# Performance work log

Measured on AMD Instinct MI355X. Metric: run time of the kernel, lower is better.

The kernel has to match this reference:

```python
import jax, jax.numpy as jnp
import numpy as np

NUM_GRAPHS = 256


def _mean_aggregate(h, src, dst, num_nodes):
    # DGL copy_src + mean reduce: dst node gets mean of src-node features over in-edges.
    summed = jax.ops.segment_sum(h[src], dst, num_segments=num_nodes)  # [N, F]
    deg = jax.ops.segment_sum(jnp.ones((src.shape[0],), h.dtype), dst, num_segments=num_nodes)
    return summed / jnp.maximum(deg, 1.0)[:, None]


def setup_inputs() -> dict:
    key = jax.random.key(0)
    ks = jax.random.split(key, 10)
    N, E, D_IN, H1, H2, OUT = 50000, 800000, 128, 256, 128, 1
    s = lambda fan: 1.0 / np.sqrt(fan)
    return {
        "h": jax.random.normal(ks[0], (N, D_IN), jnp.float32),
        "src": jax.random.randint(ks[1], (E,), 0, N),
        "dst": jax.random.randint(ks[2], (E,), 0, N),
        "graph_ids": jnp.sort(jax.random.randint(ks[3], (N,), 0, NUM_GRAPHS)),
        "W1": jax.random.normal(ks[4], (D_IN, H1), jnp.float32) * s(D_IN),
        "b1": jnp.zeros((H1,), jnp.float32),
        "W2": jax.random.normal(ks[5], (H1, H1), jnp.float32) * s(H1),
        "b2": jnp.zeros((H1,), jnp.float32),
        "Wr1": jax.random.normal(ks[6], (H1, H2), jnp.float32) * s(H1),
        "br1": jnp.zeros((H2,), jnp.float32),
        "Wr2": jax.random.normal(ks[7], (H2, OUT), jnp.float32) * s(H2),
        "br2": jnp.zeros((OUT,), jnp.float32),
    }


def reference(h, src, dst, graph_ids, W1, b1, W2, b2, Wr1, br1, Wr2, br2):
    N = h.shape[0]
    # GCN layer 1: mean-aggregate then linear+ReLU
    h = _mean_aggregate(h, src, dst, N)
    h = jax.nn.relu(h @ W1 + b1)
    # GCN layer 2
    h = _mean_aggregate(h, src, dst, N)
    h = jax.nn.relu(h @ W2 + b2)
    # dgl.mean_nodes readout: per-graph mean of node features
    gsum = jax.ops.segment_sum(h, graph_ids, num_segments=NUM_GRAPHS)  # [G, H1]
    gcnt = jax.ops.segment_sum(jnp.ones((N,), h.dtype), graph_ids, num_segments=NUM_GRAPHS)
    hg = gsum / jnp.maximum(gcnt, 1.0)[:, None]
    hidden = hg @ Wr1 + br1
    return hidden @ Wr2 + br2  # [G, 1]
```

## Files before the change

### kernel.cpp

```cpp
#include <hip/hip_runtime.h>


#define NUM_GRAPHS 256
#define MAXDEG 64
#define GSHIFT 9
#define GCAP 9216

#define PART_B0 0
#define PART_NB 256
#define CST_B0 (PART_B0 + PART_NB)
#define CST_NB 512
#define GST_B0 (CST_B0 + CST_NB)
#define GST_NB 64
#define WT1_B0 (GST_B0 + GST_NB)
#define WT1_NB 16
#define WT2_B0 (WT1_B0 + WT1_NB)
#define WT2_NB 32
#define MISC_NB (WT2_B0 + WT2_NB)

typedef __attribute__((ext_vector_type(8))) short bf16x8;
typedef __attribute__((ext_vector_type(4))) float f32x4;

__device__ inline unsigned short f2bf(float f) {
    unsigned u = __float_as_uint(f);
    return (unsigned short)((u + 0x7fff + ((u >> 16) & 1)) >> 16);
}
__device__ inline float bflo(unsigned u) { return __uint_as_float(u << 16); }
__device__ inline float bfhi(unsigned u) { return __uint_as_float(u & 0xffff0000u); }


__launch_bounds__(256)
__global__ void misc_kernel(const int* __restrict__ dst, const int* __restrict__ src,
                            const int* __restrict__ gids,
                            const float* __restrict__ h,
                            const float* __restrict__ W1, const float* __restrict__ W2,
                            int* __restrict__ cursor, unsigned* __restrict__ partE,
                            int* __restrict__ gstart,
                            unsigned short* __restrict__ hb,
                            unsigned short* __restrict__ Wt1, unsigned short* __restrict__ Wt2,
                            int N, int E) {
    int b = blockIdx.x, tid = threadIdx.x;
    if (b < CST_B0) {
        __shared__ unsigned lcnt[128];
        __shared__ unsigned gb[128];
        int ngrp = (N + 511) >> GSHIFT;
        int b0 = b - PART_B0;
        int chunk = (E + PART_NB - 1) / PART_NB;
        int ebeg = b0 * chunk;
        int eend = ebeg + chunk; if (eend > E) eend = E;
        for (int i = tid; i < 128; i += 256) lcnt[i] = 0;
        __syncthreads();
        for (int e = ebeg + tid; e < eend; e += 256) {
            int d = __builtin_nontemporal_load(&dst[e]);
            atomicAdd(&lcnt[d >> GSHIFT], 1u);
        }
        __syncthreads();
        for (int g = tid; g < ngrp; g += 256) {
            unsigned c = lcnt[g];
            gb[g] = c ? (unsigned)atomicAdd(&cursor[g], (int)c) : 0u;
            lcnt[g] = 0;
        }
        __syncthreads();
        for (int e = ebeg + tid; e < eend; e += 256) {
            int d = __builtin_nontemporal_load(&dst[e]);
            int s = __builtin_nontemporal_load(&src[e]);
            int g = d >> GSHIFT;
            unsigned r = atomicAdd(&lcnt[g], 1u) + gb[g];
            if (r < GCAP)
                __builtin_nontemporal_store(((unsigned)s << GSHIFT) | (unsigned)(d & 511),
                                            &partE[(size_t)g * GCAP + r]);
        }
    } else if (b < GST_B0) {
        int lid = (b - CST_B0) * 256 + tid;
        int total4 = N * 32;
        for (int i = lid; i < total4; i += CST_NB * 256) {
            float4 v = *(const float4*)(h + (size_t)i * 4);
            ushort4 o;
            o.x = f2bf(v.x); o.y = f2bf(v.y); o.z = f2bf(v.z); o.w = f2bf(v.w);
            *(ushort4*)(hb + (size_t)i * 4) = o;
        }
    } else if (b < WT1_B0) {
        int lid = (b - GST_B0) * 256 + tid;
        for (int n = lid; n < N; n += GST_NB * 256) {
            int g = gids[n];
            int gp = (n == 0) ? -1 : gids[n - 1];
            for (int x = gp + 1; x <= g; ++x) gstart[x] = n;
            if (n == N - 1)
                for (int x = g + 1; x <= NUM_GRAPHS; ++x) gstart[x] = N;
        }
    } else if (b < WT2_B0) {
        int lid = (b - WT1_B0) * 256 + tid;
        for (int i = lid; i < 256 * 128; i += WT1_NB * 256)
            Wt1[i] = f2bf(W1[(size_t)(i & 127) * 256 + (i >> 7)]);
    } else {
        int lid = (b - WT2_B0) * 256 + tid;
        for (int i = lid; i < 256 * 256; i += WT2_NB * 256)
            Wt2[i] = f2bf(W2[(size_t)(i & 255) * 256 + (i >> 8)]);
    }
}


__launch_bounds__(256)
__global__ void build_kernel(const unsigned* __restrict__ partE,
                             const int* __restrict__ cursor,
                             int* __restrict__ cnt, unsigned short* __restrict__ eidx,
                             int N) {
    __shared__ unsigned hist[512];
    int g = blockIdx.x, tid = threadIdx.x;
    for (int i = tid; i < 512; i += 256) hist[i] = 0;
    __syncthreads();
    int ec = cursor[g]; if (ec > GCAP) ec = GCAP;
    const unsigned* pe = partE + (size_t)g * GCAP;
    for (int i = tid; i < ec; i += 256) {
        unsigned p = pe[i];
        int dl = (int)(p & 511);
        int s = (int)(p >> GSHIFT);
        unsigned r = atomicAdd(&hist[dl], 1u);
        if (r < MAXDEG)
            eidx[((size_t)((g << GSHIFT) + dl)) * MAXDEG + r] = (unsigned short)s;
    }
    __syncthreads();
    for (int i = tid; i < 512; i += 256) {
        int node = (g << GSHIFT) + i;
        if (node < N) cnt[node] = (int)hist[i];
    }
}


template <int D>
__global__ void agg_mean_bf16_kernel(const unsigned short* __restrict__ feat,
                                     const int* __restrict__ cnt,
                                     const unsigned short* __restrict__ eidx,
                                     unsigned short* __restrict__ out, int N) {
    constexpr int VPL = D / 64;
    int wave = blockIdx.x * (blockDim.x >> 6) + (threadIdx.x >> 6);
    int lane = threadIdx.x & 63;
    if (wave >= N) return;
    int deg = cnt[wave];
    int stored = deg > MAXDEG ? MAXDEG : deg;
    const unsigned short* row = eidx + (size_t)wave * MAXDEG;
    int myIdx = (lane < stored) ? (int)row[lane] : 0;

    float acc[VPL];
    #pragma unroll
    for (int i = 0; i < VPL; ++i) acc[i] = 0.0f;

    int j = 0;
    for (; j + 8 <= stored; j += 8) {
        if constexpr (VPL == 2) {
            unsigned v[8];
            #pragma unroll
            for (int u = 0; u < 8; ++u) {
                int s = __shfl(myIdx, j + u, 64);
                v[u] = *(const unsigned*)(feat + (size_t)s * D + lane * 2);
            }
            #pragma unroll
            for (int u = 0; u < 8; ++u) { acc[0] += bflo(v[u]); acc[1] += bfhi(v[u]); }
        } else {
            uint2 v[8];
            #pragma unroll
            for (int u = 0; u < 8; ++u) {
                int s = __shfl(myIdx, j + u, 64);
                v[u] = *(const uint2*)(feat + (size_t)s * D + lane * 4);
            }
            #pragma unroll
            for (int u = 0; u < 8; ++u) {
                acc[0] += bflo(v[u].x); acc[1] += bfhi(v[u].x);
                acc[2] += bflo(v[u].y); acc[3] += bfhi(v[u].y);
            }
        }
    }
    for (; j < stored; ++j) {
        int s = __shfl(myIdx, j, 64);
        if constexpr (VPL == 2) {
            unsigned v = *(const unsigned*)(feat + (size_t)s * D + lane * 2);
            acc[0] += bflo(v); acc[1] += bfhi(v);
        } else {
            uint2 v = *(const uint2*)(feat + (size_t)s * D + lane * 4);
            acc[0] += bflo(v.x); acc[1] += bfhi(v.x);
            acc[2] += bflo(v.y); acc[3] += bfhi(v.y);
        }
    }

    float invd = 1.0f / (float)(deg > 0 ? deg : 1);
    if constexpr (VPL == 2) {
        unsigned o = (unsigned)f2bf(acc[0] * invd) | ((unsigned)f2bf(acc[1] * invd) << 16);
        __builtin_nontemporal_store(o, (unsigned*)(out + (size_t)wave * D + lane * 2));
    } else {
        unsigned lo = (unsigned)f2bf(acc[0] * invd) | ((unsigned)f2bf(acc[1] * invd) << 16);
        unsigned hi = (unsigned)f2bf(acc[2] * invd) | ((unsigned)f2bf(acc[3] * invd) << 16);
        unsigned long long o = (unsigned long long)lo | ((unsigned long long)hi << 32);
        __builtin_nontemporal_store(o, (unsigned long long*)(out + (size_t)wave * D + lane * 4));
    }
}


template <int K, int MODE>
__launch_bounds__(256)
__global__ void gemm_mfma_kernel(const unsigned short* __restrict__ A,
                                 const unsigned short* __restrict__ Wt,
                                 const float* __restrict__ bias,
                                 unsigned short* __restrict__ Cb,
                                 const int* __restrict__ gids,
                                 float* __restrict__ gsum,
                                 int N) {
    constexpr int LDS = 40;
    __shared__ unsigned short As[64 * LDS];
    __shared__ unsigned short Bs[256 * LDS];

    int tid = threadIdx.x;
    int wave = tid >> 6;
    int lane = tid & 63;
    int m = lane & 15;
    int q = lane >> 4;
    int rowBase = blockIdx.x * 64;

    f32x4 acc[4][4] = {};

    for (int kc = 0; kc < K; kc += 32) {
        {
            int r = tid >> 2;
            int seg = tid & 3;
            int gr = rowBase + r;
            uint4 v = make_uint4(0, 0, 0, 0);
            if (gr < N) v = *(const uint4*)(A + (size_t)gr * K + kc + seg * 8);
            *(uint4*)&As[r * LDS + seg * 8] = v;
        }
        #pragma unroll
        for (int it = 0; it < 4; ++it) {
            int n = (tid >> 2) + it * 64;
            int seg = tid & 3;
            uint4 v = *(const uint4*)(Wt + (size_t)n * K + kc + seg * 8);
            *(uint4*)&Bs[n * LDS + seg * 8] = v;
        }
        __syncthreads();

        bf16x8 af[4], bfr[4];
        #pragma unroll
        for (int r = 0; r < 4; ++r)
            af[r] = *(const bf16x8*)&As[(r * 16 + m) * LDS + q * 8];
        #pragma unroll
        for (int c = 0; c < 4; ++c)
            bfr[c] = *(const bf16x8*)&Bs[(wave * 64 + c * 16 + m) * LDS + q * 8];
        #pragma unroll
        for (int r = 0; r < 4; ++r)
            #pragma unroll
            for (int c = 0; c < 4; ++c)
                acc[r][c] = __builtin_amdgcn_mfma_f32_16x16x32_bf16(af[r], bfr[c], acc[r][c], 0, 0, 0);
        __syncthreads();
    }

    if constexpr (MODE == 0) {
        #pragma unroll
        for (int c = 0; c < 4; ++c) {
            int col = wave * 64 + c * 16 + m;
            float bv = bias[col];
            #pragma unroll
            for (int r = 0; r < 4; ++r) {
                #pragma unroll
                for (int reg = 0; reg < 4; ++reg) {
                    int grow = rowBase + r * 16 + q * 4 + reg;
                    if (grow < N)
                        Cb[(size_t)grow * 256 + col] = f2bf(fmaxf(acc[r][c][reg] + bv, 0.0f));
                }
            }
        }
    } else {
        int* sgid = (int*)As;
        if (tid < 64) {
            int gr = rowBase + tid;
            sgid[tid] = (gr < N) ? gids[gr] : 0x7fffffff;
        }
        __syncthreads();
        int lastValid = N - 1 - rowBase;
        if (lastValid > 63) lastValid = 63;
        int gmin = sgid[0];
        int gmax = sgid[lastValid];
        #pragma unroll
        for (int c = 0; c < 4; ++c) {
            int col = wave * 64 + c * 16 + m;
            float bv = bias[col];
            for (int g = gmin; g <= gmax; ++g) {
                float p = 0.0f;
                #pragma unroll
                for (int r = 0; r < 4; ++r) {
                    #pragma unroll
                    for (int reg = 0; reg < 4; ++reg) {
                        int lr = r * 16 + q * 4 + reg;
                        if (sgid[lr] == g)
                            p += fmaxf(acc[r][c][reg] + bv, 0.0f);
                    }
                }
                p += __shfl_xor(p, 16, 64);
                p += __shfl_xor(p, 32, 64);
                if (q == 0 && p != 0.0f)
                    atomicAdd(&gsum[g * 256 + col], p);
            }
        }
    }
}


__global__ void final_kernel(const float* __restrict__ gsum, const int* __restrict__ gstart,
                             const float* __restrict__ Wr1, const float* __restrict__ br1,
                             const float* __restrict__ Wr2, const float* __restrict__ br2,
                             float* __restrict__ out) {
    __shared__ float part[512];
    __shared__ float ws2[2];
    int g = blockIdx.x;
    int t = threadIdx.x;
    int j = t & 127;
    int kq = t >> 7;
    int c = gstart[g + 1] - gstart[g];
    float invc = 1.0f / (float)(c > 0 ? c : 1);
    const float* gs = gsum + g * 256;
    float acc = 0.0f;
    #pragma unroll 8
    for (int k = kq * 64; k < kq * 64 + 64; ++k)
        acc += gs[k] * Wr1[k * 128 + j];
    part[t] = acc;
    __syncthreads();
    if (t < 128) {
        float s = part[j] + part[128 + j] + part[256 + j] + part[384 + j];
        float p = (s * invc + br1[j]) * Wr2[j];
        #pragma unroll
        for (int d = 32; d > 0; d >>= 1) p += __shfl_down(p, d, 64);
        if ((t & 63) == 0) ws2[t >> 6] = p;
    }
    __syncthreads();
    if (t == 0) out[g] = ws2[0] + ws2[1] + br2[0];
}


extern "C" void kernel_launch(void* const* d_in, const int* in_sizes, int n_in,
                              void* d_out, int out_size, void* d_ws, size_t ws_size,
                              hipStream_t stream) {
    const float* h    = (const float*)d_in[0];
    const int*   src  = (const int*)d_in[1];
    const int*   dst  = (const int*)d_in[2];
    const int*   gids = (const int*)d_in[3];
    const float* W1   = (const float*)d_in[4];
    const float* b1   = (const float*)d_in[5];
    const float* W2   = (const float*)d_in[6];
    const float* b2   = (const float*)d_in[7];
    const float* Wr1  = (const float*)d_in[8];
    const float* br1  = (const float*)d_in[9];
    const float* Wr2  = (const float*)d_in[10];
    const float* br2  = (const float*)d_in[11];

    int N = in_sizes[0] / 128;
    int E = in_sizes[1];
    int ngrp = (N + 511) >> GSHIFT;

    char* w = (char*)d_ws;
    unsigned short* hb     = (unsigned short*)w;  w += (size_t)N * 128 * sizeof(unsigned short);
    unsigned short* h1b    = (unsigned short*)w;  w += (size_t)N * 256 * sizeof(unsigned short);
    unsigned short* aggOut = (unsigned short*)w;  w += (size_t)N * 256 * sizeof(unsigned short);
    int* cnt    = (int*)w;              w += (size_t)N * sizeof(int);
    float* gsum = (float*)w;            w += (size_t)NUM_GRAPHS * 256 * sizeof(float);
    int* cursor = (int*)w;              w += 128 * sizeof(int);
    unsigned short* eidx = (unsigned short*)w;  w += (size_t)N * MAXDEG * sizeof(unsigned short);
    unsigned short* Wt1 = (unsigned short*)w;   w += 256 * 128 * sizeof(unsigned short);
    unsigned short* Wt2 = (unsigned short*)w;   w += 256 * 256 * sizeof(unsigned short);
    int* gstart = (int*)w;              w += (size_t)(NUM_GRAPHS + 1) * sizeof(int);
    unsigned* partE = (unsigned*)aggOut;

    hipMemsetAsync(gsum, 0,
                   (size_t)NUM_GRAPHS * 256 * sizeof(float) + 128 * sizeof(int),
                   stream);
    misc_kernel<<<MISC_NB, 256, 0, stream>>>(dst, src, gids, h, W1, W2, cursor, partE,
                                             gstart, hb, Wt1, Wt2, N, E);
    build_kernel<<<ngrp, 256, 0, stream>>>(partE, cursor, cnt, eidx, N);

    agg_mean_bf16_kernel<128><<<(N + 3) / 4, 256, 0, stream>>>(hb, cnt, eidx, aggOut, N);
    gemm_mfma_kernel<128, 0><<<(N + 63) / 64, 256, 0, stream>>>(aggOut, Wt1, b1, h1b, nullptr, nullptr, N);

    agg_mean_bf16_kernel<256><<<(N + 3) / 4, 256, 0, stream>>>(h1b, cnt, eidx, aggOut, N);
    gemm_mfma_kernel<256, 1><<<(N + 63) / 64, 256, 0, stream>>>(aggOut, Wt2, b2, nullptr, gids, gsum, N);

    final_kernel<<<NUM_GRAPHS, 512, 0, stream>>>(gsum, gstart, Wr1, br1, Wr2, br2, (float*)d_out);
}
```

Measured before the change: 286.7 us.

## Stage edge partitioning in LDS for coalesced writes and smaller dst groups

The edge partitioning pass now sorts each block's edges by destination group in shared memory, using a prefix scan and a compaction buffer, then writes them out contiguously per group instead of scattering them one by one. Groups shrink from 512 to 256 destination nodes, which doubles the number of build blocks and halves their per-group capacity. The build kernel assembles each group's neighbour lists in LDS and writes them out with vectorised nontemporal stores, replacing scattered 2-byte global writes. In exchange it adds scan barriers, a binary search per edge and 32KB of LDS in the build kernel, which may lower occupancy.

```diff
diff --git a/kernel.cpp b/kernel.cpp
--- a/kernel.cpp
+++ b/kernel.cpp
@@ -3,8 +3,9 @@
 
 #define NUM_GRAPHS 256
 #define MAXDEG 64
-#define GSHIFT 9
-#define GCAP 9216
+#define GSHIFT 8
+#define GCAP 4864
+#define CHUNK_MAX 3200
 
 #define PART_B0 0
 #define PART_NB 256
@@ -20,6 +21,7 @@
 
 typedef __attribute__((ext_vector_type(8))) short bf16x8;
 typedef __attribute__((ext_vector_type(4))) float f32x4;
+typedef __attribute__((ext_vector_type(4))) unsigned int u32x4;
 
 __device__ inline unsigned short f2bf(float f) {
     unsigned u = __float_as_uint(f);
@@ -41,34 +43,57 @@
                             int N, int E) {
     int b = blockIdx.x, tid = threadIdx.x;
     if (b < CST_B0) {
-        __shared__ unsigned lcnt[128];
-        __shared__ unsigned gb[128];
-        int ngrp = (N + 511) >> GSHIFT;
+        __shared__ unsigned lcnt[256];
+        __shared__ unsigned sbuf[256];
+        __shared__ unsigned lbase[257];
+        __shared__ unsigned gb[256];
+        __shared__ unsigned comp[CHUNK_MAX];
         int b0 = b - PART_B0;
         int chunk = (E + PART_NB - 1) / PART_NB;
         int ebeg = b0 * chunk;
         int eend = ebeg + chunk; if (eend > E) eend = E;
-        for (int i = tid; i < 128; i += 256) lcnt[i] = 0;
+        int ecount = eend - ebeg; if (ecount < 0) ecount = 0;
+
+        lcnt[tid] = 0;
         __syncthreads();
         for (int e = ebeg + tid; e < eend; e += 256) {
             int d = __builtin_nontemporal_load(&dst[e]);
             atomicAdd(&lcnt[d >> GSHIFT], 1u);
         }
         __syncthreads();
-        for (int g = tid; g < ngrp; g += 256) {
-            unsigned c = lcnt[g];
-            gb[g] = c ? (unsigned)atomicAdd(&cursor[g], (int)c) : 0u;
-            lcnt[g] = 0;
-        }
+        unsigned v = lcnt[tid];
+        sbuf[tid] = v;
+        __syncthreads();
+        #pragma unroll
+        for (int dd = 1; dd < 256; dd <<= 1) {
+            unsigned t = (tid >= dd) ? sbuf[tid - dd] : 0u;
+            __syncthreads();
+            sbuf[tid] += t;
+            __syncthreads();
+        }
+        lbase[tid] = sbuf[tid] - v;
+        if (tid == 255) lbase[256] = sbuf[255];
+        gb[tid] = v ? (unsigned)atomicAdd(&cursor[tid], (int)v) : 0u;
+        lcnt[tid] = 0;
         __syncthreads();
         for (int e = ebeg + tid; e < eend; e += 256) {
             int d = __builtin_nontemporal_load(&dst[e]);
             int s = __builtin_nontemporal_load(&src[e]);
             int g = d >> GSHIFT;
-            unsigned r = atomicAdd(&lcnt[g], 1u) + gb[g];
-            if (r < GCAP)
-                __builtin_nontemporal_store(((unsigned)s << GSHIFT) | (unsigned)(d & 511),
-                                            &partE[(size_t)g * GCAP + r]);
+            unsigned r = atomicAdd(&lcnt[g], 1u) + lbase[g];
+            if (r < (unsigned)CHUNK_MAX)
+                comp[r] = ((unsigned)s << GSHIFT) | (unsigned)(d & 255);
+        }
+        __syncthreads();
+        for (int i = tid; i < ecount; i += 256) {
+            int lo = 0, hi = 256;
+            while (hi - lo > 1) {
+                int mid = (lo + hi) >> 1;
+                if (lbase[mid] <= (unsigned)i) lo = mid; else hi = mid;
+            }
+            unsigned dest = (unsigned)lo * GCAP + gb[lo] + ((unsigned)i - lbase[lo]);
+            if (dest < (unsigned)(256 * GCAP))
+                __builtin_nontemporal_store(comp[i], &partE[dest]);
         }
     } else if (b < GST_B0) {
         int lid = (b - CST_B0) * 256 + tid;
@@ -105,25 +130,28 @@
                              const int* __restrict__ cursor,
                              int* __restrict__ cnt, unsigned short* __restrict__ eidx,
                              int N) {
-    __shared__ unsigned hist[512];
+    __shared__ unsigned short es[256 * MAXDEG];
+    __shared__ unsigned hist[256];
     int g = blockIdx.x, tid = threadIdx.x;
-    for (int i = tid; i < 512; i += 256) hist[i] = 0;
+    hist[tid] = 0;
     __syncthreads();
     int ec = cursor[g]; if (ec > GCAP) ec = GCAP;
     const unsigned* pe = partE + (size_t)g * GCAP;
     for (int i = tid; i < ec; i += 256) {
         unsigned p = pe[i];
-        int dl = (int)(p & 511);
+        int dl = (int)(p & 255);
         int s = (int)(p >> GSHIFT);
         unsigned r = atomicAdd(&hist[dl], 1u);
         if (r < MAXDEG)
-            eidx[((size_t)((g << GSHIFT) + dl)) * MAXDEG + r] = (unsigned short)s;
+            es[dl * MAXDEG + r] = (unsigned short)s;
     }
     __syncthreads();
-    for (int i = tid; i < 512; i += 256) {
-        int node = (g << GSHIFT) + i;
-        if (node < N) cnt[node] = (int)hist[i];
-    }
+    const u32x4* s4 = (const u32x4*)es;
+    u32x4* d4 = (u32x4*)(eidx + ((size_t)g << GSHIFT) * MAXDEG);
+    for (int i = tid; i < 2048; i += 256)
+        __builtin_nontemporal_store(s4[i], &d4[i]);
+    int node = (g << GSHIFT) + tid;
+    if (node < N) cnt[node] = (int)hist[tid];
 }
 
 
@@ -350,7 +378,7 @@
 
     int N = in_sizes[0] / 128;
     int E = in_sizes[1];
-    int ngrp = (N + 511) >> GSHIFT;
+    int ngrp = (N + 255) >> GSHIFT;
 
     char* w = (char*)d_ws;
     unsigned short* hb     = (unsigned short*)w;  w += (size_t)N * 128 * sizeof(unsigned short);
@@ -358,16 +386,16 @@
     unsigned short* aggOut = (unsigned short*)w;  w += (size_t)N * 256 * sizeof(unsigned short);
     int* cnt    = (int*)w;              w += (size_t)N * sizeof(int);
     float* gsum = (float*)w;            w += (size_t)NUM_GRAPHS * 256 * sizeof(float);
-    int* cursor = (int*)w;              w += 128 * sizeof(int);
-    unsigned short* eidx = (unsigned short*)w;  w += (size_t)N * MAXDEG * sizeof(unsigned short);
+    int* cursor = (int*)w;              w += 256 * sizeof(int);
+    unsigned short* eidx = (unsigned short*)w;  w += (size_t)ngrp * 256 * MAXDEG * sizeof(unsigned short);
     unsigned short* Wt1 = (unsigned short*)w;   w += 256 * 128 * sizeof(unsigned short);
     unsigned short* Wt2 = (unsigned short*)w;   w += 256 * 256 * sizeof(unsigned short);
     int* gstart = (int*)w;              w += (size_t)(NUM_GRAPHS + 1) * sizeof(int);
     unsigned* partE = (unsigned*)aggOut;
 
-    hipMemsetAsync(gsum, 0,
-                   (size_t)NUM_GRAPHS * 256 * sizeof(float) + 128 * sizeof(int),
-                   stream);
+    (void)hipMemsetAsync(gsum, 0,
+                         (size_t)NUM_GRAPHS * 256 * sizeof(float) + 256 * sizeof(int),
+                         stream);
     misc_kernel<<<MISC_NB, 256, 0, stream>>>(dst, src, gids, h, W1, W2, cursor, partE,
                                              gstart, hb, Wt1, Wt2, N, E);
     build_kernel<<<ngrp, 256, 0, stream>>>(partE, cursor, cnt, eidx, N);
```

Measured after the change: 279.4 us (median of 2 runs). 2.6% less time.
